# Optimization experiments

Hardware: AMD Instinct MI355X
Metric: run time of the kernel (lower is better)

The kernel has to match this reference:

```python
import jax, jax.numpy as jnp
import numpy as np

IN_DIM = 8192   # input feature dim (kernel rows)
OUT_DIM = 8192  # output_sz (kernel cols, number of LIF neurons)
INIT_TAU = 2.0  # learnable tau logit; leak = sigmoid(INIT_TAU)
V_TH = 1.0      # v_threshold


def setup_inputs() -> dict:
    key = jax.random.key(0)
    k1, k2 = jax.random.split(key, 2)
    x = jax.random.normal(k1, (IN_DIM,), jnp.float32)
    W = jax.random.normal(k2, (IN_DIM, OUT_DIM), jnp.float32) / np.float32(np.sqrt(IN_DIM))
    b = jnp.zeros((OUT_DIM,), jnp.float32)
    u = jnp.zeros((OUT_DIM,), jnp.float32)       # membrane potential carry
    a_hat = jnp.zeros((IN_DIM,), jnp.float32)    # presynaptic eligibility trace carry
    return {"W": W, "b": b, "u": u, "a_hat": a_hat, "x": x}


def reference(W, b, u, a_hat, x):
    # One OTTT step: dense projection + leaky-integrate-fire + spike + trace update.
    sig_tau = jax.nn.sigmoid(INIT_TAU)
    u_pre = sig_tau * u + x @ W + b          # leaky integrate
    s = (u_pre >= V_TH).astype(W.dtype)      # spike (heaviside)
    u_new = u_pre - s * V_TH                 # soft reset
    a_hat_new = sig_tau * a_hat + x          # online eligibility trace: a_hat = sig_tau*a_hat + inputs
    return s, u_new, a_hat_new
```

## Files before the change

kernel.cpp:

```cpp
#include <hip/hip_runtime.h>


#define IN_DIM   8192
#define OUT_DIM  8192
#define SIG_TAU  0.8807970779778823f
#define V_TH     1.0f

__global__ __launch_bounds__(256) void gemv_partial(
    const float* __restrict__ W,
    const float* __restrict__ x,
    float* __restrict__ part,
    int chunk_rows)
{
    const int col4 = blockIdx.x * blockDim.x + threadIdx.x;
    const int row0 = blockIdx.y * chunk_rows;

    extern __shared__ float xs[];
    for (int t = threadIdx.x; t < chunk_rows; t += blockDim.x)
        xs[t] = x[row0 + t];
    __syncthreads();

    const float4* Wp = (const float4*)W + (size_t)row0 * (OUT_DIM / 4) + col4;
    float4 acc = make_float4(0.f, 0.f, 0.f, 0.f);

    #pragma unroll 4
    for (int r = 0; r < chunk_rows; ++r) {
        float4 w = Wp[(size_t)r * (OUT_DIM / 4)];
        float xv = xs[r];
        acc.x = fmaf(xv, w.x, acc.x);
        acc.y = fmaf(xv, w.y, acc.y);
        acc.z = fmaf(xv, w.z, acc.z);
        acc.w = fmaf(xv, w.w, acc.w);
    }

    ((float4*)part)[(size_t)blockIdx.y * (OUT_DIM / 4) + col4] = acc;
}

__global__ __launch_bounds__(256) void finalize_lif(
    const float* __restrict__ part,
    const float* __restrict__ b,
    const float* __restrict__ u,
    const float* __restrict__ a_hat,
    const float* __restrict__ x,
    float* __restrict__ out,
    int nchunks)
{
    const int j = blockIdx.x * blockDim.x + threadIdx.x;
    if (j >= OUT_DIM) return;

    float sum = 0.f;
    for (int c = 0; c < nchunks; ++c)
        sum += part[(size_t)c * OUT_DIM + j];

    const float u_pre = fmaf(SIG_TAU, u[j], sum + b[j]);
    const float s = (u_pre >= V_TH) ? 1.0f : 0.0f;

    out[j]               = s;
    out[OUT_DIM + j]     = u_pre - s * V_TH;
    out[2 * OUT_DIM + j] = fmaf(SIG_TAU, a_hat[j], x[j]);
}

extern "C" void kernel_launch(void* const* d_in, const int* in_sizes, int n_in,
                              void* d_out, int out_size, void* d_ws, size_t ws_size,
                              hipStream_t stream)
{
    const float* W     = (const float*)d_in[0];
    const float* b     = (const float*)d_in[1];
    const float* u     = (const float*)d_in[2];
    const float* a_hat = (const float*)d_in[3];
    const float* x     = (const float*)d_in[4];
    float* out  = (float*)d_out;
    float* part = (float*)d_ws;

    int nchunks = 128;
    while (nchunks > 1 && (size_t)nchunks * OUT_DIM * sizeof(float) > ws_size)
        nchunks >>= 1;
    const int chunk_rows = IN_DIM / nchunks;

    dim3 grid(OUT_DIM / (4 * 256), nchunks);
    gemv_partial<<<grid, 256, chunk_rows * sizeof(float), stream>>>(W, x, part, chunk_rows);

    finalize_lif<<<OUT_DIM / 256, 256, 0, stream>>>(part, b, u, a_hat, x, out, nchunks);
}
```

Measured before the change: 395.6 us.

## Restructure GEMV into row-slab blocks with two-level partial-sum reduction

```diff
diff --git a/kernel.cpp b/kernel.cpp
--- a/kernel.cpp
+++ b/kernel.cpp
@@ -3,40 +3,124 @@
 
 #define IN_DIM   8192
 #define OUT_DIM  8192
+#define COLS4    (OUT_DIM / 4)
 #define SIG_TAU  0.8807970779778823f
 #define V_TH     1.0f
 
-__global__ __launch_bounds__(256) void gemv_partial(
+#define ROWS_PB  16
+#define NCH      (IN_DIM / ROWS_PB)
+#define GROUPS   16
+#define CH_PER_G (NCH / GROUPS)
+#define TILES    8
+
+__global__ __launch_bounds__(256, 2) void gemv_slab(
+    const float* __restrict__ W,
+    const float* __restrict__ x,
+    float* __restrict__ part)
+{
+    const int row0 = blockIdx.x * ROWS_PB;
+
+    __shared__ float xs[ROWS_PB];
+    if (threadIdx.x < ROWS_PB) xs[threadIdx.x] = x[row0 + threadIdx.x];
+    __syncthreads();
+
+    float xv[ROWS_PB];
+    #pragma unroll
+    for (int r = 0; r < ROWS_PB; ++r) xv[r] = xs[r];
+
+    const float4* Wp = (const float4*)W + (size_t)row0 * COLS4 + threadIdx.x;
+
+    float4 acc[TILES];
+    #pragma unroll
+    for (int t = 0; t < TILES; ++t) acc[t] = make_float4(0.f, 0.f, 0.f, 0.f);
+
+    #pragma unroll 4
+    for (int r = 0; r < ROWS_PB; ++r) {
+        #pragma unroll
+        for (int t = 0; t < TILES; ++t) {
+            float4 w = Wp[(size_t)r * COLS4 + t * 256];
+            acc[t].x = fmaf(xv[r], w.x, acc[t].x);
+            acc[t].y = fmaf(xv[r], w.y, acc[t].y);
+            acc[t].z = fmaf(xv[r], w.z, acc[t].z);
+            acc[t].w = fmaf(xv[r], w.w, acc[t].w);
+        }
+    }
+
+    float4* pp = (float4*)part + (size_t)blockIdx.x * COLS4 + threadIdx.x;
+    #pragma unroll
+    for (int t = 0; t < TILES; ++t) pp[t * 256] = acc[t];
+}
+
+__global__ __launch_bounds__(256) void reduce_a(
+    const float* __restrict__ part,
+    float* __restrict__ part2)
+{
+    const int col = blockIdx.x * 256 + threadIdx.x;
+    const int g   = blockIdx.y;
+    const float* p = part + (size_t)g * CH_PER_G * OUT_DIM + col;
+
+    float s = 0.f;
+    #pragma unroll
+    for (int c = 0; c < CH_PER_G; ++c)
+        s += p[(size_t)c * OUT_DIM];
+
+    part2[(size_t)g * OUT_DIM + col] = s;
+}
+
+__global__ __launch_bounds__(256) void finalize_lif2(
+    const float* __restrict__ part2,
+    const float* __restrict__ b,
+    const float* __restrict__ u,
+    const float* __restrict__ a_hat,
+    const float* __restrict__ x,
+    float* __restrict__ out)
+{
+    const int j = blockIdx.x * 256 + threadIdx.x;
+
+    float sum = 0.f;
+    #pragma unroll
+    for (int g = 0; g < GROUPS; ++g)
+        sum += part2[(size_t)g * OUT_DIM + j];
+
+    const float u_pre = fmaf(SIG_TAU, u[j], sum + b[j]);
+    const float s = (u_pre >= V_TH) ? 1.0f : 0.0f;
+
+    out[j]               = s;
+    out[OUT_DIM + j]     = u_pre - s * V_TH;
+    out[2 * OUT_DIM + j] = fmaf(SIG_TAU, a_hat[j], x[j]);
+}
+
+__global__ __launch_bounds__(256) void gemv_partial_gen(
     const float* __restrict__ W,
     const float* __restrict__ x,
     float* __restrict__ part,
     int chunk_rows)
 {
-    const int col4 = blockIdx.x * blockDim.x + threadIdx.x;
+    const int col4 = blockIdx.x * 256 + threadIdx.x;
     const int row0 = blockIdx.y * chunk_rows;
 
-    extern __shared__ float xs[];
-    for (int t = threadIdx.x; t < chunk_rows; t += blockDim.x)
-        xs[t] = x[row0 + t];
+    extern __shared__ float xsg[];
+    for (int t = threadIdx.x; t < chunk_rows; t += 256)
+        xsg[t] = x[row0 + t];
     __syncthreads();
 
-    const float4* Wp = (const float4*)W + (size_t)row0 * (OUT_DIM / 4) + col4;
+    const float4* Wp = (const float4*)W + (size_t)row0 * COLS4 + col4;
     float4 acc = make_float4(0.f, 0.f, 0.f, 0.f);
 
-    #pragma unroll 4
+    #pragma unroll 8
     for (int r = 0; r < chunk_rows; ++r) {
-        float4 w = Wp[(size_t)r * (OUT_DIM / 4)];
-        float xv = xs[r];
-        acc.x = fmaf(xv, w.x, acc.x);
-        acc.y = fmaf(xv, w.y, acc.y);
-        acc.z = fmaf(xv, w.z, acc.z);
-        acc.w = fmaf(xv, w.w, acc.w);
+        float4 w = Wp[(size_t)r * COLS4];
+        const float xvv = xsg[r];
+        acc.x = fmaf(xvv, w.x, acc.x);
+        acc.y = fmaf(xvv, w.y, acc.y);
+        acc.z = fmaf(xvv, w.z, acc.z);
+        acc.w = fmaf(xvv, w.w, acc.w);
     }
 
-    ((float4*)part)[(size_t)blockIdx.y * (OUT_DIM / 4) + col4] = acc;
+    ((float4*)part)[(size_t)blockIdx.y * COLS4 + col4] = acc;
 }
 
-__global__ __launch_bounds__(256) void finalize_lif(
+__global__ __launch_bounds__(256) void finalize_lif1(
     const float* __restrict__ part,
     const float* __restrict__ b,
     const float* __restrict__ u,
@@ -45,10 +129,11 @@
     float* __restrict__ out,
     int nchunks)
 {
-    const int j = blockIdx.x * blockDim.x + threadIdx.x;
+    const int j = blockIdx.x * 256 + threadIdx.x;
     if (j >= OUT_DIM) return;
 
     float sum = 0.f;
+    #pragma unroll 8
     for (int c = 0; c < nchunks; ++c)
         sum += part[(size_t)c * OUT_DIM + j];
 
@@ -69,16 +154,27 @@
     const float* u     = (const float*)d_in[2];
     const float* a_hat = (const float*)d_in[3];
     const float* x     = (const float*)d_in[4];
-    float* out  = (float*)d_out;
-    float* part = (float*)d_ws;
+    float* out = (float*)d_out;
 
-    int nchunks = 128;
-    while (nchunks > 1 && (size_t)nchunks * OUT_DIM * sizeof(float) > ws_size)
-        nchunks >>= 1;
-    const int chunk_rows = IN_DIM / nchunks;
+    const size_t part_elems  = (size_t)NCH * OUT_DIM;
+    const size_t part2_elems = (size_t)GROUPS * OUT_DIM;
 
-    dim3 grid(OUT_DIM / (4 * 256), nchunks);
-    gemv_partial<<<grid, 256, chunk_rows * sizeof(float), stream>>>(W, x, part, chunk_rows);
+    if ((part_elems + part2_elems) * sizeof(float) <= ws_size) {
+        float* part  = (float*)d_ws;
+        float* part2 = part + part_elems;
 
-    finalize_lif<<<OUT_DIM / 256, 256, 0, stream>>>(part, b, u, a_hat, x, out, nchunks);
+        gemv_slab<<<NCH, 256, 0, stream>>>(W, x, part);
+        dim3 ga(OUT_DIM / 256, GROUPS);
+        reduce_a<<<ga, 256, 0, stream>>>(part, part2);
+        finalize_lif2<<<OUT_DIM / 256, 256, 0, stream>>>(part2, b, u, a_hat, x, out);
+    } else {
+        float* part = (float*)d_ws;
+        int nchunks = 128;
+        while (nchunks > 1 && (size_t)nchunks * OUT_DIM * sizeof(float) > ws_size)
+            nchunks >>= 1;
+        const int chunk_rows = IN_DIM / nchunks;
+        dim3 grid(OUT_DIM / (4 * 256), nchunks);
+        gemv_partial_gen<<<grid, 256, chunk_rows * sizeof(float), stream>>>(W, x, part, chunk_rows);
+        finalize_lif1<<<OUT_DIM / 256, 256, 0, stream>>>(part, b, u, a_hat, x, out, nchunks);
+    }
 }
```

Measured after the change: 380.2 us. 1.04x faster.
